# Kernel tuning notes

Measured on AMD Instinct MI355X. Metric: run time of the kernel, lower is better.

## Reference

```python
import jax, jax.numpy as jnp
import numpy as np


def setup_inputs() -> dict:
    key = jax.random.key(0)
    kK, kP, ki, ke = jax.random.split(key, 4)
    B, n = 512, 4096
    K_batch = jax.random.normal(kK, (B, n), dtype=jnp.float32)
    # Phi must be symmetric PSD (the module treats it as a kernel/metric matrix:
    # grad of sum(R@A*R) is written as 2*R@A, valid only for symmetric A).
    W = jax.random.normal(kP, (n, n), dtype=jnp.float32) / np.float32(np.sqrt(n))
    Phi = W @ W.T  # eigenvalues O(1)
    imp = jax.random.normal(ki, (1024,), dtype=jnp.float32)
    exc = jax.random.normal(ke, (1024,), dtype=jnp.float32)
    a = jnp.float32(1.0)
    gamma = jnp.float32(1.0)
    return {"K_batch": K_batch, "a": a, "exc": exc, "imp": imp,
            "Phi": Phi, "gamma": gamma}


def reference(K_batch, a, exc, imp, Phi, gamma):
    """OptNet-style layer: solve, per sample i,
         min_r  (gamma/B)*||r||^2 + ((||imp||^2+||exc||^2)/B) * r^T Phi r
         s.t.   a * <r, k_i> = 1
    Closed-form KKT solution (what the original SPG iteration converges to):
         r_i = M^{-1} k_i / (a * k_i^T M^{-1} k_i),
         M   = (gamma/B) I + ((||imp||^2+||exc||^2)/B) Phi.
    """
    B, n = K_batch.shape
    imp2 = jnp.sum(imp * imp)   # ||imp||^2
    exc2 = jnp.sum(exc * exc)   # ||exc||^2
    M = (imp2 + exc2) / B * Phi + (gamma / B) * jnp.eye(n, dtype=K_batch.dtype)
    # z_i = M^{-1} k_i for all samples at once: solve with B right-hand sides.
    Z = jnp.linalg.solve(M, K_batch.T).T            # [B, n]
    denom = a * jnp.sum(Z * K_batch, axis=1)        # [B], = a * k_i^T M^{-1} k_i
    opt_x = Z / denom[:, None]                      # [B, n]
    return opt_x
```

## Files before the change

### kernel.cpp

```cpp
#include <hip/hip_runtime.h>


#define N    4096
#define NRHS 512
#define NB   128
#define PSTR 68
#define DSTR 136
#define TSTR 136
#define BSTR 68

__device__ __forceinline__ int xcd_map(int bid, int nwg) {
  int x = bid & 7, i = bid >> 3;
  int q = nwg >> 3, r = nwg & 7;
  return (x < r ? x * (q + 1) : r * (q + 1) + (x - r) * q) + i;
}

template<int S>
__device__ __forceinline__ void asm_levelA(float* __restrict__ sh, int tid) {
  constexpr int TOT = (64 / S) * S * (S / 4);
  constexpr int F4 = S / 4;
  for (int id = tid; id < TOT; id += 512) {
    int pair = id / (S * F4);
    int rem = id - pair * (S * F4);
    int r = rem / F4, c4 = rem - r * F4;
    int o = 2 * S * pair;
    const float* arow = &sh[(o + S + r) * DSTR + o];
    float4 a4 = {0.f, 0.f, 0.f, 0.f};
    for (int t = 0; t < S; ++t) {
      float a = arow[t];
      const float4 b = *(const float4*)&sh[(o + t) * DSTR + o + 4 * c4];
      a4.x += a * b.x; a4.y += a * b.y; a4.z += a * b.z; a4.w += a * b.w;
    }
    *(float4*)&sh[(S * pair + r) * DSTR + 64 + 4 * c4] = a4;
  }
}
template<int S>
__device__ __forceinline__ void asm_levelB(float* __restrict__ sh, int tid) {
  constexpr int TOT = (64 / S) * S * (S / 4);
  constexpr int F4 = S / 4;
  for (int id = tid; id < TOT; id += 512) {
    int pair = id / (S * F4);
    int rem = id - pair * (S * F4);
    int r = rem / F4, c4 = rem - r * F4;
    int o = 2 * S * pair;
    const float* u2row = &sh[(o + S + r) * DSTR + o + S];
    float4 a4 = {0.f, 0.f, 0.f, 0.f};
    for (int t = 0; t < S; ++t) {
      float a = u2row[t];
      const float4 w = *(const float4*)&sh[(S * pair + t) * DSTR + 64 + 4 * c4];
      a4.x += a * w.x; a4.y += a * w.y; a4.z += a * w.z; a4.w += a * w.w;
    }
    float4 ov = {-a4.x, -a4.y, -a4.z, -a4.w};
    *(float4*)&sh[(o + S + r) * DSTR + o + 4 * c4] = ov;
  }
}

__global__ __launch_bounds__(256) void k_scalars(const float* __restrict__ imp,
                                                 const float* __restrict__ exc,
                                                 const float* __restrict__ gamma,
                                                 float* __restrict__ c) {
  __shared__ float red[256];
  int tid = threadIdx.x;
  float s = 0.0f;
  for (int i = tid; i < 1024; i += 256) { float x = imp[i], y = exc[i]; s += x * x + y * y; }
  red[tid] = s; __syncthreads();
  for (int w = 128; w > 0; w >>= 1) { if (tid < w) red[tid] += red[tid + w]; __syncthreads(); }
  if (tid == 0) { c[0] = red[0] / 512.0f; c[1] = gamma[0] / 512.0f; }
}

__global__ __launch_bounds__(256) void k_build_M(const float* __restrict__ Phi,
                                                 const float* __restrict__ c,
                                                 float* __restrict__ M) {
  int idx = blockIdx.x * 256 + threadIdx.x;
  int base = idx * 4;
  float4 p = *(const float4*)(Phi + base);
  float c1 = c[0], c2 = c[1];
  float4 m;
  m.x = c1 * p.x; m.y = c1 * p.y; m.z = c1 * p.z; m.w = c1 * p.w;
  int r = base >> 12, c0 = base & (N - 1);
  if (r == c0)     m.x += c2;
  if (r == c0 + 1) m.y += c2;
  if (r == c0 + 2) m.z += c2;
  if (r == c0 + 3) m.w += c2;
  *(float4*)(M + base) = m;
}

__global__ __launch_bounds__(256) void k_transpose(const float* __restrict__ K,
                                                   float* __restrict__ S) {
  __shared__ float t[32][33];
  int bi = blockIdx.x, bb = blockIdx.y;
  int tx = threadIdx.x & 31, ty = threadIdx.x >> 5;
  for (int r = 0; r < 4; ++r)
    t[ty + 8 * r][tx] = K[(size_t)(bb * 32 + ty + 8 * r) * N + bi * 32 + tx];
  __syncthreads();
  for (int r = 0; r < 4; ++r)
    S[(size_t)(bi * 32 + ty + 8 * r) * NRHS + bb * 32 + tx] = t[tx][ty + 8 * r];
}

__global__ __launch_bounds__(512, 2) void k_syrk_potrf(float* __restrict__ M,
                                                       float* __restrict__ U,
                                                       int kdiag, int k0) {
  __shared__ float sh[NB * DSTR];
  __shared__ float dinv[NB];
  float* Pa = sh;
  float* Pb = sh + NB * PSTR;
  int tid = threadIdx.x;
  int p = (gridDim.x > 1) ? xcd_map(blockIdx.x, gridDim.x) : 0;
  int g4 = tid >> 4;
  int cm = tid & 15;
  int rr4 = g4 * 4;

  if (p > 0) {
    int br = (int)((sqrtf(8.f * (float)p + 1.f) - 1.f) * 0.5f);
    while (((br + 1) * (br + 2)) / 2 <= p) ++br;
    while ((br * (br + 1)) / 2 > p) --br;
    int bc = p - (br * (br + 1)) / 2;
    int t0k = kdiag * NB;
    int r0 = t0k + br * NB, c0 = t0k + bc * NB;
    float acc[4][8] = {};
    for (int ch = 0; ch < 2; ++ch) {
      int kc = k0 + ch * 64;
      __syncthreads();
#pragma unroll
      for (int i = 0; i < 4; ++i) {
        int idx = tid + (i << 9);
        int r = idx >> 4, f4 = idx & 15;
        *(float4*)&Pa[r * PSTR + 4 * f4] = *(const float4*)(M + (size_t)(r0 + r) * N + kc + 4 * f4);
        *(float4*)&Pb[r * PSTR + 4 * f4] = *(const float4*)(M + (size_t)(c0 + r) * N + kc + 4 * f4);
      }
      __syncthreads();
#pragma unroll 2
      for (int tc = 0; tc < 64; tc += 4) {
        float4 a4[4], b4[8];
#pragma unroll
        for (int q = 0; q < 4; ++q) a4[q] = *(const float4*)&Pa[(rr4 + ((q + g4) & 3)) * PSTR + tc];
#pragma unroll
        for (int w = 0; w < 8; ++w) b4[w] = *(const float4*)&Pb[(cm + 16 * w) * PSTR + tc];
#pragma unroll
        for (int q = 0; q < 4; ++q)
#pragma unroll
          for (int w = 0; w < 8; ++w)
            acc[q][w] += a4[q].x * b4[w].x + a4[q].y * b4[w].y
                       + a4[q].z * b4[w].z + a4[q].w * b4[w].w;
      }
    }
    for (int q = 0; q < 4; ++q) {
      int row = r0 + rr4 + ((q + g4) & 3);
      float* mp = M + (size_t)row * N + c0 + cm;
#pragma unroll
      for (int w = 0; w < 8; ++w) mp[16 * w] -= acc[q][w];
    }
    return;
  }

  int kr = kdiag * NB;
  float acc[4][8] = {};
  if (k0 >= 0) {
    for (int ch = 0; ch < 2; ++ch) {
      int kc = k0 + ch * 64;
      __syncthreads();
#pragma unroll
      for (int i = 0; i < 4; ++i) {
        int idx = tid + (i << 9);
        int r = idx >> 4, f4 = idx & 15;
        *(float4*)&Pa[r * PSTR + 4 * f4] = *(const float4*)(M + (size_t)(kr + r) * N + kc + 4 * f4);
      }
      __syncthreads();
#pragma unroll 2
      for (int tc = 0; tc < 64; tc += 4) {
        float4 a4[4], b4[8];
#pragma unroll
        for (int q = 0; q < 4; ++q) a4[q] = *(const float4*)&Pa[(rr4 + ((q + g4) & 3)) * PSTR + tc];
#pragma unroll
        for (int w = 0; w < 8; ++w) b4[w] = *(const float4*)&Pa[(cm + 16 * w) * PSTR + tc];
#pragma unroll
        for (int q = 0; q < 4; ++q)
#pragma unroll
          for (int w = 0; w < 8; ++w)
            acc[q][w] += a4[q].x * b4[w].x + a4[q].y * b4[w].y
                       + a4[q].z * b4[w].z + a4[q].w * b4[w].w;
      }
    }
  }
  __syncthreads();
#pragma unroll
  for (int e = 0; e < 8; ++e) {
    int idx = tid + (e << 9);
    int r = idx >> 5, f4 = idx & 31;
    *(float4*)&sh[r * DSTR + 4 * f4] = *(const float4*)(M + (size_t)(kr + r) * N + kr + 4 * f4);
  }
  __syncthreads();
#pragma unroll
  for (int q = 0; q < 4; ++q) {
    int row = rr4 + ((q + g4) & 3);
#pragma unroll
    for (int w = 0; w < 8; ++w) {
      int col = cm + 16 * w;
      if ((row >> 4) < (col >> 4)) sh[row * DSTR + col] = 0.0f;
      else if (k0 >= 0) sh[row * DSTR + col] -= acc[q][w];
    }
  }
  __syncthreads();

#pragma unroll 1
  for (int pp = 0; pp < 8; ++pp) {
    const int b0 = 16 * pp;
    if (tid < 16) {
      int l = tid;
      float r[16];
#pragma unroll
      for (int t = 0; t < 16; ++t) r[t] = sh[(b0 + l) * DSTR + b0 + t];
#pragma unroll
      for (int j = 0; j < 16; ++j) {
        float d = __shfl(r[j], j);
        float inv = rsqrtf(d);
        if (l == j) r[j] = d * inv;
        else if (l > j) r[j] *= inv;
        if (l == 0) dinv[b0 + j] = inv;
#pragma unroll
        for (int t = j + 1; t < 16; ++t) {
          float Ltj = __shfl(r[j], t);
          if (l >= t) r[t] -= r[j] * Ltj;
        }
      }
#pragma unroll
      for (int t = 0; t < 16; ++t) if (t <= l) sh[(b0 + l) * DSTR + b0 + t] = r[t];
    }
    __syncthreads();
    const int base = b0 + 16, nbl = NB - base;
    if (nbl > 0) {
      if (tid < nbl) {
        const int rg = base + tid;
        float xr[16];
#pragma unroll
        for (int j = 0; j < 16; ++j) {
          float v = sh[rg * DSTR + b0 + j];
#pragma unroll
          for (int t = 0; t < 16; ++t)
            if (t < j) v -= xr[t] * sh[(b0 + j) * DSTR + b0 + t];
          xr[j] = v * dinv[b0 + j];
          sh[rg * DSTR + b0 + j] = xr[j];
        }
      }
      __syncthreads();
      for (int i = tid >> 3; i < nbl; i += 64) {
        const float* ai = &sh[(base + i) * DSTR + b0];
        float4 a0 = *(const float4*)ai,       a1 = *(const float4*)(ai + 4);
        float4 a2 = *(const float4*)(ai + 8), a3 = *(const float4*)(ai + 12);
        for (int j = tid & 7; j <= i; j += 8) {
          const float* bj = &sh[(base + j) * DSTR + b0];
          float4 c0 = *(const float4*)bj,       c1 = *(const float4*)(bj + 4);
          float4 c2 = *(const float4*)(bj + 8), c3 = *(const float4*)(bj + 12);
          float s = a0.x*c0.x + a0.y*c0.y + a0.z*c0.z + a0.w*c0.w
                  + a1.x*c1.x + a1.y*c1.y + a1.z*c1.z + a1.w*c1.w
                  + a2.x*c2.x + a2.y*c2.y + a2.z*c2.z + a2.w*c2.w
                  + a3.x*c3.x + a3.y*c3.y + a3.z*c3.z + a3.w*c3.w;
          sh[(base + i) * DSTR + base + j] -= s;
        }
      }
      __syncthreads();
    }
  }

  if (tid < 128) {
    const int g = tid >> 4, l = tid & 15, b0 = 16 * g;
    float x[16];
#pragma unroll
    for (int i = 0; i < 16; ++i) {
      float s = (l == i) ? 1.0f : 0.0f;
#pragma unroll
      for (int t = 0; t < 16; ++t)
        if (t < i) s -= sh[(b0 + i) * DSTR + b0 + t] * x[t];
      x[i] = s * dinv[b0 + i];
      sh[(b0 + i) * DSTR + b0 + l] = x[i];
    }
  }
  __syncthreads();

  asm_levelA<16>(sh, tid); __syncthreads();
  asm_levelB<16>(sh, tid); __syncthreads();
  asm_levelA<32>(sh, tid); __syncthreads();
  asm_levelB<32>(sh, tid); __syncthreads();
  asm_levelA<64>(sh, tid); __syncthreads();
  asm_levelB<64>(sh, tid); __syncthreads();

#pragma unroll
  for (int e = 0; e < 8; ++e) {
    int idx = tid + (e << 9);
    int i = idx >> 5, f4 = idx & 31;
    float4 v;
    if ((i >> 4) >= (f4 >> 2)) v = *(const float4*)&sh[i * DSTR + 4 * f4];
    else v = make_float4(0.f, 0.f, 0.f, 0.f);
    *(float4*)(U + (size_t)i * NB + 4 * f4) = v;
  }
}

__global__ __launch_bounds__(512, 2) void k_trsm(float* __restrict__ M,
                                                 const float* __restrict__ Ug, int k0) {
  __shared__ float Pa[NB * PSTR];
  __shared__ float Pb[NB * PSTR];
  int tid = threadIdx.x;
  int g4 = tid >> 4, rr4 = g4 * 4, cm = tid & 15;
  int r0 = k0 + NB + blockIdx.x * NB;
  float acc[4][8] = {};
  for (int ch = 0; ch < 2; ++ch) {
    int kc = k0 + ch * 64;
    __syncthreads();
#pragma unroll
    for (int i = 0; i < 4; ++i) {
      int idx = tid + (i << 9);
      int r = idx >> 4, f4 = idx & 15;
      *(float4*)&Pa[r * PSTR + 4 * f4] = *(const float4*)(M + (size_t)(r0 + r) * N + kc + 4 * f4);
      *(float4*)&Pb[r * PSTR + 4 * f4] = *(const float4*)(Ug + (size_t)r * NB + ch * 64 + 4 * f4);
    }
    __syncthreads();
#pragma unroll 2
    for (int tc = 0; tc < 64; tc += 4) {
      float4 a4[4], b4[8];
#pragma unroll
      for (int q = 0; q < 4; ++q) a4[q] = *(const float4*)&Pa[(rr4 + ((q + g4) & 3)) * PSTR + tc];
#pragma unroll
      for (int w = 0; w < 8; ++w) b4[w] = *(const float4*)&Pb[(cm + 16 * w) * PSTR + tc];
#pragma unroll
      for (int q = 0; q < 4; ++q)
#pragma unroll
        for (int w = 0; w < 8; ++w)
          acc[q][w] += a4[q].x * b4[w].x + a4[q].y * b4[w].y
                     + a4[q].z * b4[w].z + a4[q].w * b4[w].w;
    }
  }
  for (int q = 0; q < 4; ++q) {
    int row = r0 + rr4 + ((q + g4) & 3);
    float* mp = M + (size_t)row * N + k0 + cm;
#pragma unroll
    for (int w = 0; w < 8; ++w) mp[16 * w] = acc[q][w];
  }
}

__global__ __launch_bounds__(256) void k_fsolve(float* __restrict__ S,
                                                float* __restrict__ X,
                                                const float* __restrict__ M,
                                                const float* __restrict__ Uk,
                                                int k0) {
  __shared__ float Xl[NB][BSTR];
  __shared__ float Aa[16][TSTR];
  __shared__ float Bb[16][BSTR];
  int tid = threadIdx.x;
  int id = xcd_map(blockIdx.x, gridDim.x);
  int d = id >> 3;
  int b0 = (id & 7) * 64;
  int i0g = k0 + d * NB;
  int ii = (tid >> 3) * 4, bl = (tid & 7) * 8;
  float acc[4][8] = {};
  for (int tch = 0; tch < NB; tch += 16) {
#pragma unroll
    for (int it = 0; it < 2; ++it) {
      int idx = tid + it * 256;
      int j = idx >> 2, f4 = idx & 3;
      const float4 v = *(const float4*)(Uk + (size_t)j * NB + tch + 4 * f4);
      Aa[4 * f4 + 0][j] = v.x; Aa[4 * f4 + 1][j] = v.y;
      Aa[4 * f4 + 2][j] = v.z; Aa[4 * f4 + 3][j] = v.w;
    }
    {
      int t = tid >> 4, f = tid & 15;
      *(float4*)&Bb[t][4 * f] = *(const float4*)(S + (size_t)(k0 + tch + t) * NRHS + b0 + 4 * f);
    }
    __syncthreads();
#pragma unroll 4
    for (int t = 0; t < 16; ++t) {
      float4 a0 = *(const float4*)&Aa[t][ii];
      float4 b0v = *(const float4*)&Bb[t][bl];
      float4 b1v = *(const float4*)&Bb[t][bl + 4];
      float av[4] = {a0.x, a0.y, a0.z, a0.w};
      float bv[8] = {b0v.x, b0v.y, b0v.z, b0v.w, b1v.x, b1v.y, b1v.z, b1v.w};
#pragma unroll
      for (int q = 0; q < 4; ++q)
#pragma unroll
        for (int w = 0; w < 8; ++w) acc[q][w] += av[q] * bv[w];
    }
    __syncthreads();
  }
  if (d == 0) {
    for (int q = 0; q < 4; ++q) {
      float* xp = X + (size_t)(k0 + ii + q) * NRHS + b0 + bl;
      float4 x0 = {acc[q][0], acc[q][1], acc[q][2], acc[q][3]};
      float4 x1 = {acc[q][4], acc[q][5], acc[q][6], acc[q][7]};
      *(float4*)xp = x0; *((float4*)xp + 1) = x1;
    }
    return;
  }
  for (int q = 0; q < 4; ++q) {
    float4 x0 = {acc[q][0], acc[q][1], acc[q][2], acc[q][3]};
    float4 x1 = {acc[q][4], acc[q][5], acc[q][6], acc[q][7]};
    *(float4*)&Xl[ii + q][bl] = x0; *(float4*)&Xl[ii + q][bl + 4] = x1;
  }
  __syncthreads();
  float acc2[4][8] = {};
  for (int tch = 0; tch < NB; tch += 16) {
    for (int idx = tid; idx < 512; idx += 256) {
      int r = idx >> 2, q = idx & 3;
      const float4 v = *(const float4*)(M + (size_t)(i0g + r) * N + k0 + tch + 4 * q);
      Aa[4 * q + 0][r] = v.x; Aa[4 * q + 1][r] = v.y;
      Aa[4 * q + 2][r] = v.z; Aa[4 * q + 3][r] = v.w;
    }
    __syncthreads();
#pragma unroll 4
    for (int t = 0; t < 16; ++t) {
      float4 a0 = *(const float4*)&Aa[t][ii];
      float4 b0v = *(const float4*)&Xl[tch + t][bl];
      float4 b1v = *(const float4*)&Xl[tch + t][bl + 4];
      float av[4] = {a0.x, a0.y, a0.z, a0.w};
      float bv[8] = {b0v.x, b0v.y, b0v.z, b0v.w, b1v.x, b1v.y, b1v.z, b1v.w};
#pragma unroll
      for (int q = 0; q < 4; ++q)
#pragma unroll
        for (int w = 0; w < 8; ++w) acc2[q][w] += av[q] * bv[w];
    }
    __syncthreads();
  }
  for (int q = 0; q < 4; ++q) {
    float* sp = S + (size_t)(i0g + ii + q) * NRHS + b0 + bl;
    float4 x0 = *(float4*)sp, x1 = *((float4*)sp + 1);
    x0.x -= acc2[q][0]; x0.y -= acc2[q][1]; x0.z -= acc2[q][2]; x0.w -= acc2[q][3];
    x1.x -= acc2[q][4]; x1.y -= acc2[q][5]; x1.z -= acc2[q][6]; x1.w -= acc2[q][7];
    *(float4*)sp = x0; *((float4*)sp + 1) = x1;
  }
}

__global__ __launch_bounds__(256) void k_bsolve(float* __restrict__ X,
                                                float* __restrict__ S,
                                                const float* __restrict__ M,
                                                const float* __restrict__ Uk,
                                                int k0) {
  __shared__ float Xl[NB][BSTR];
  __shared__ float Aa[16][TSTR];
  __shared__ float Bb[16][BSTR];
  int tid = threadIdx.x;
  int id = xcd_map(blockIdx.x, gridDim.x);
  int d = id >> 3;
  int b0 = (id & 7) * 64;
  int i0g = k0 - d * NB;
  int ii = (tid >> 3) * 4, bl = (tid & 7) * 8;
  float acc[4][8] = {};
  for (int tch = 0; tch < NB; tch += 16) {
    for (int idx = tid; idx < 512; idx += 256) {
      int t = idx >> 5, f = idx & 31;
      *(float4*)&Aa[t][4 * f] = *(const float4*)(Uk + (size_t)(tch + t) * NB + 4 * f);
    }
    {
      int t = tid >> 4, f = tid & 15;
      *(float4*)&Bb[t][4 * f] = *(const float4*)(X + (size_t)(k0 + tch + t) * NRHS + b0 + 4 * f);
    }
    __syncthreads();
#pragma unroll 4
    for (int t = 0; t < 16; ++t) {
      float4 a0 = *(const float4*)&Aa[t][ii];
      float4 b0v = *(const float4*)&Bb[t][bl];
      float4 b1v = *(const float4*)&Bb[t][bl + 4];
      float av[4] = {a0.x, a0.y, a0.z, a0.w};
      float bv[8] = {b0v.x, b0v.y, b0v.z, b0v.w, b1v.x, b1v.y, b1v.z, b1v.w};
#pragma unroll
      for (int q = 0; q < 4; ++q)
#pragma unroll
        for (int w = 0; w < 8; ++w) acc[q][w] += av[q] * bv[w];
    }
    __syncthreads();
  }
  if (d == 0) {
    for (int q = 0; q < 4; ++q) {
      float* sp = S + (size_t)(k0 + ii + q) * NRHS + b0 + bl;
      float4 x0 = {acc[q][0], acc[q][1], acc[q][2], acc[q][3]};
      float4 x1 = {acc[q][4], acc[q][5], acc[q][6], acc[q][7]};
      *(float4*)sp = x0; *((float4*)sp + 1) = x1;
    }
    return;
  }
  for (int q = 0; q < 4; ++q) {
    float4 x0 = {acc[q][0], acc[q][1], acc[q][2], acc[q][3]};
    float4 x1 = {acc[q][4], acc[q][5], acc[q][6], acc[q][7]};
    *(float4*)&Xl[ii + q][bl] = x0; *(float4*)&Xl[ii + q][bl + 4] = x1;
  }
  __syncthreads();
  float acc2[4][8] = {};
  for (int tch = 0; tch < NB; tch += 16) {
    for (int idx = tid; idx < 512; idx += 256) {
      int t = idx >> 5, f = idx & 31;
      *(float4*)&Aa[t][4 * f] = *(const float4*)(M + (size_t)(k0 + tch + t) * N + i0g + 4 * f);
    }
    __syncthreads();
#pragma unroll 4
    for (int t = 0; t < 16; ++t) {
      float4 a0 = *(const float4*)&Aa[t][ii];
      float4 b0v = *(const float4*)&Xl[tch + t][bl];
      float4 b1v = *(const float4*)&Xl[tch + t][bl + 4];
      float av[4] = {a0.x, a0.y, a0.z, a0.w};
      float bv[8] = {b0v.x, b0v.y, b0v.z, b0v.w, b1v.x, b1v.y, b1v.z, b1v.w};
#pragma unroll
      for (int q = 0; q < 4; ++q)
#pragma unroll
        for (int w = 0; w < 8; ++w) acc2[q][w] += av[q] * bv[w];
    }
    __syncthreads();
  }
  for (int q = 0; q < 4; ++q) {
    float* xp = X + (size_t)(i0g + ii + q) * NRHS + b0 + bl;
    float4 x0 = *(float4*)xp, x1 = *((float4*)xp + 1);
    x0.x -= acc2[q][0]; x0.y -= acc2[q][1]; x0.z -= acc2[q][2]; x0.w -= acc2[q][3];
    x1.x -= acc2[q][4]; x1.y -= acc2[q][5]; x1.z -= acc2[q][6]; x1.w -= acc2[q][7];
    *(float4*)xp = x0; *((float4*)xp + 1) = x1;
  }
}

__global__ __launch_bounds__(256) void k_final(const float* __restrict__ S,
                                               const float* __restrict__ K,
                                               const float* __restrict__ a_ptr,
                                               float* __restrict__ out) {
  __shared__ float red[256];
  int b = blockIdx.x, tid = threadIdx.x;
  float s = 0.0f;
  for (int i = tid; i < N; i += 256) s += S[(size_t)i * NRHS + b] * K[(size_t)b * N + i];
  red[tid] = s; __syncthreads();
  for (int w = 128; w > 0; w >>= 1) { if (tid < w) red[tid] += red[tid + w]; __syncthreads(); }
  float inv = 1.0f / (a_ptr[0] * red[0]);
  for (int i = tid; i < N; i += 256) out[(size_t)b * N + i] = S[(size_t)i * NRHS + b] * inv;
}

extern "C" void kernel_launch(void* const* d_in, const int* in_sizes, int n_in,
                              void* d_out, int out_size, void* d_ws, size_t ws_size,
                              hipStream_t stream) {
  const float* Kb    = (const float*)d_in[0];
  const float* a     = (const float*)d_in[1];
  const float* exc   = (const float*)d_in[2];
  const float* imp   = (const float*)d_in[3];
  const float* Phi   = (const float*)d_in[4];
  const float* gamma = (const float*)d_in[5];
  float* out = (float*)d_out;

  float* M  = (float*)d_ws;
  float* S  = M + (size_t)N * N;
  float* X  = S + (size_t)N * NRHS;
  float* U  = X + (size_t)N * NRHS;
  float* c  = U + (size_t)32 * NB * NB;

  k_scalars<<<1, 256, 0, stream>>>(imp, exc, gamma, c);
  k_build_M<<<N * N / 1024, 256, 0, stream>>>(Phi, c, M);
  k_transpose<<<dim3(N / 32, NRHS / 32), 256, 0, stream>>>(Kb, S);

  k_syrk_potrf<<<1, 512, 0, stream>>>(M, U, 0, -1);
  for (int k = 0; k <= 30; ++k) {
    int k0 = k * NB;
    k_trsm<<<31 - k, 512, 0, stream>>>(M, U + (size_t)k * NB * NB, k0);
    int T = 31 - k;
    int pairs = (T * (T + 1)) / 2;
    k_syrk_potrf<<<pairs, 512, 0, stream>>>(M, U + (size_t)(k + 1) * NB * NB, k + 1, k0);
  }
  for (int k = 0; k < 32; ++k)
    k_fsolve<<<8 * (32 - k), 256, 0, stream>>>(S, X, M, U + (size_t)k * NB * NB, k * NB);
  for (int k = 31; k >= 0; --k)
    k_bsolve<<<8 * (k + 1), 256, 0, stream>>>(X, S, M, U + (size_t)k * NB * NB, k * NB);
  k_final<<<NRHS, 256, 0, stream>>>(S, Kb, a, out);
}
```

Baseline: 4.976 ms.

## Use 32-wide panels in diagonal-block Cholesky and overlap next corner factor with trailing update

The in-LDS factorization of each 128x128 diagonal block now works on 32-column panels instead of 16. Each step runs the next panel's corner factorization on one wavefront while the other threads apply the remaining trailing update in parallel. The diagonal-block inverse starts from 32x32 blocks, which removes the 16-level assembly passes. The goal is fewer barriers and less serial work on the critical path per block. The cost is larger per-thread register arrays (32 floats) and longer serial triangular solves per thread.

New measurement: 5.319 ms. 6.9% more time.

```diff
diff --git a/kernel.cpp b/kernel.cpp
--- a/kernel.cpp
+++ b/kernel.cpp
@@ -55,6 +55,42 @@
   }
 }
 
+__device__ __forceinline__ void corner_factor32(float* __restrict__ sh,
+                                                float* __restrict__ dinv,
+                                                int c0, int l) {
+  float r[32];
+#pragma unroll
+  for (int t = 0; t < 32; ++t) r[t] = sh[(c0 + l) * DSTR + c0 + t];
+#pragma unroll
+  for (int j = 0; j < 32; ++j) {
+    float d = __shfl(r[j], j);
+    float inv = rsqrtf(d);
+    if (l == j) r[j] = d * inv;
+    else if (l > j) r[j] *= inv;
+    if (l == 0) dinv[c0 + j] = inv;
+#pragma unroll
+    for (int t = j + 1; t < 32; ++t) {
+      float Ltj = __shfl(r[j], t);
+      if (l >= t) r[t] -= r[j] * Ltj;
+    }
+  }
+#pragma unroll
+  for (int t = 0; t < 32; ++t) if (t <= l) sh[(c0 + l) * DSTR + c0 + t] = r[t];
+}
+
+__device__ __forceinline__ float dot32(const float* __restrict__ sh, int i, int j, int b0) {
+  const float* ai = &sh[i * DSTR + b0];
+  const float* bj = &sh[j * DSTR + b0];
+  float s = 0.0f;
+#pragma unroll
+  for (int q = 0; q < 8; ++q) {
+    float4 a = *(const float4*)(ai + 4 * q);
+    float4 b = *(const float4*)(bj + 4 * q);
+    s += a.x * b.x + a.y * b.y + a.z * b.z + a.w * b.w;
+  }
+  return s;
+}
+
 __global__ __launch_bounds__(256) void k_scalars(const float* __restrict__ imp,
                                                  const float* __restrict__ exc,
                                                  const float* __restrict__ gamma,
@@ -202,83 +238,65 @@
   }
   __syncthreads();
 
+  if (tid < 32) corner_factor32(sh, dinv, 0, tid);
+  __syncthreads();
 #pragma unroll 1
-  for (int pp = 0; pp < 8; ++pp) {
-    const int b0 = 16 * pp;
-    if (tid < 16) {
-      int l = tid;
-      float r[16];
-#pragma unroll
-      for (int t = 0; t < 16; ++t) r[t] = sh[(b0 + l) * DSTR + b0 + t];
-#pragma unroll
-      for (int j = 0; j < 16; ++j) {
-        float d = __shfl(r[j], j);
-        float inv = rsqrtf(d);
-        if (l == j) r[j] = d * inv;
-        else if (l > j) r[j] *= inv;
-        if (l == 0) dinv[b0 + j] = inv;
-#pragma unroll
-        for (int t = j + 1; t < 16; ++t) {
-          float Ltj = __shfl(r[j], t);
-          if (l >= t) r[t] -= r[j] * Ltj;
+  for (int pp = 0; pp < 3; ++pp) {
+    const int b0 = 32 * pp;
+    const int base = b0 + 32;
+    const int nbl = NB - base;
+    if (tid < nbl) {
+      const int rg = base + tid;
+      float xr[32];
+#pragma unroll
+      for (int j = 0; j < 32; ++j) {
+        float v = sh[rg * DSTR + b0 + j];
+#pragma unroll
+        for (int t = 0; t < 32; ++t)
+          if (t < j) v -= xr[t] * sh[(b0 + j) * DSTR + b0 + t];
+        xr[j] = v * dinv[b0 + j];
+        sh[rg * DSTR + b0 + j] = xr[j];
+      }
+    }
+    __syncthreads();
+    for (int e = tid; e < 1024; e += 512) {
+      int i = base + (e >> 5), j = base + (e & 31);
+      if (j <= i) sh[i * DSTR + j] -= dot32(sh, i, j, b0);
+    }
+    __syncthreads();
+    if (tid < 32) {
+      corner_factor32(sh, dinv, base, tid);
+    } else if (tid >= 64) {
+      const int base2 = base + 32;
+      const int nb2 = NB - base2;
+      if (nb2 > 0) {
+        const int ncol = NB - base;
+        const int tot = nb2 * ncol;
+        for (int e = tid - 64; e < tot; e += 448) {
+          int i = base2 + e / ncol;
+          int j = base + (e - (e / ncol) * ncol);
+          if (j <= i) sh[i * DSTR + j] -= dot32(sh, i, j, b0);
         }
       }
-#pragma unroll
-      for (int t = 0; t < 16; ++t) if (t <= l) sh[(b0 + l) * DSTR + b0 + t] = r[t];
-    }
-    __syncthreads();
-    const int base = b0 + 16, nbl = NB - base;
-    if (nbl > 0) {
-      if (tid < nbl) {
-        const int rg = base + tid;
-        float xr[16];
-#pragma unroll
-        for (int j = 0; j < 16; ++j) {
-          float v = sh[rg * DSTR + b0 + j];
-#pragma unroll
-          for (int t = 0; t < 16; ++t)
-            if (t < j) v -= xr[t] * sh[(b0 + j) * DSTR + b0 + t];
-          xr[j] = v * dinv[b0 + j];
-          sh[rg * DSTR + b0 + j] = xr[j];
-        }
-      }
-      __syncthreads();
-      for (int i = tid >> 3; i < nbl; i += 64) {
-        const float* ai = &sh[(base + i) * DSTR + b0];
-        float4 a0 = *(const float4*)ai,       a1 = *(const float4*)(ai + 4);
-        float4 a2 = *(const float4*)(ai + 8), a3 = *(const float4*)(ai + 12);
-        for (int j = tid & 7; j <= i; j += 8) {
-          const float* bj = &sh[(base + j) * DSTR + b0];
-          float4 c0 = *(const float4*)bj,       c1 = *(const float4*)(bj + 4);
-          float4 c2 = *(const float4*)(bj + 8), c3 = *(const float4*)(bj + 12);
-          float s = a0.x*c0.x + a0.y*c0.y + a0.z*c0.z + a0.w*c0.w
-                  + a1.x*c1.x + a1.y*c1.y + a1.z*c1.z + a1.w*c1.w
-                  + a2.x*c2.x + a2.y*c2.y + a2.z*c2.z + a2.w*c2.w
-                  + a3.x*c3.x + a3.y*c3.y + a3.z*c3.z + a3.w*c3.w;
-          sh[(base + i) * DSTR + base + j] -= s;
-        }
-      }
-      __syncthreads();
-    }
+    }
+    __syncthreads();
   }
 
   if (tid < 128) {
-    const int g = tid >> 4, l = tid & 15, b0 = 16 * g;
-    float x[16];
-#pragma unroll
-    for (int i = 0; i < 16; ++i) {
+    const int g = tid >> 5, l = tid & 31, c0 = 32 * g;
+    float x[32];
+#pragma unroll
+    for (int i = 0; i < 32; ++i) {
       float s = (l == i) ? 1.0f : 0.0f;
 #pragma unroll
-      for (int t = 0; t < 16; ++t)
-        if (t < i) s -= sh[(b0 + i) * DSTR + b0 + t] * x[t];
-      x[i] = s * dinv[b0 + i];
-      sh[(b0 + i) * DSTR + b0 + l] = x[i];
-    }
-  }
-  __syncthreads();
-
-  asm_levelA<16>(sh, tid); __syncthreads();
-  asm_levelB<16>(sh, tid); __syncthreads();
+      for (int t = 0; t < 32; ++t)
+        if (t < i) s -= sh[(c0 + i) * DSTR + c0 + t] * x[t];
+      x[i] = s * dinv[c0 + i];
+      sh[(c0 + i) * DSTR + c0 + l] = x[i];
+    }
+  }
+  __syncthreads();
+
   asm_levelA<32>(sh, tid); __syncthreads();
   asm_levelB<32>(sh, tid); __syncthreads();
   asm_levelA<64>(sh, tid); __syncthreads();
```

## Fuse triangular solve sweeps into persistent cooperative kernels with grid sync

Applied to the files above, without the earlier changes.

Replaces the 32 forward and 32 backward solve launches with one cooperative kernel each, which loops over block steps and uses grid.sync between them. Blocks that have no work at a given step stay idle until the next barrier. This removes per-launch overhead and launch gaps across 64 small kernels, at the cost of grid-wide barriers, a fixed 256-block grid that leaves more blocks idle in late steps, and dropping the XCD-aware block remapping.

Measured after the change: 6.724 ms. 1.35x slower.

```diff
diff --git a/kernel.cpp b/kernel.cpp
--- a/kernel.cpp
+++ b/kernel.cpp
@@ -1,4 +1,6 @@
 #include <hip/hip_runtime.h>
+#include <hip/hip_cooperative_groups.h>
+namespace cg = cooperative_groups;
 
 
 #define N    4096
@@ -337,177 +339,191 @@
   }
 }
 
-__global__ __launch_bounds__(256) void k_fsolve(float* __restrict__ S,
-                                                float* __restrict__ X,
-                                                const float* __restrict__ M,
-                                                const float* __restrict__ Uk,
-                                                int k0) {
+__global__ __launch_bounds__(256) void k_fsolve_coop(float* __restrict__ S,
+                                                     float* __restrict__ X,
+                                                     const float* __restrict__ M,
+                                                     const float* __restrict__ Uall) {
+  cg::grid_group grid = cg::this_grid();
   __shared__ float Xl[NB][BSTR];
   __shared__ float Aa[16][TSTR];
   __shared__ float Bb[16][BSTR];
   int tid = threadIdx.x;
-  int id = xcd_map(blockIdx.x, gridDim.x);
-  int d = id >> 3;
-  int b0 = (id & 7) * 64;
-  int i0g = k0 + d * NB;
+  int d = blockIdx.x >> 3;
+  int b0 = (blockIdx.x & 7) * 64;
   int ii = (tid >> 3) * 4, bl = (tid & 7) * 8;
-  float acc[4][8] = {};
-  for (int tch = 0; tch < NB; tch += 16) {
-#pragma unroll
-    for (int it = 0; it < 2; ++it) {
-      int idx = tid + it * 256;
-      int j = idx >> 2, f4 = idx & 3;
-      const float4 v = *(const float4*)(Uk + (size_t)j * NB + tch + 4 * f4);
-      Aa[4 * f4 + 0][j] = v.x; Aa[4 * f4 + 1][j] = v.y;
-      Aa[4 * f4 + 2][j] = v.z; Aa[4 * f4 + 3][j] = v.w;
-    }
-    {
-      int t = tid >> 4, f = tid & 15;
-      *(float4*)&Bb[t][4 * f] = *(const float4*)(S + (size_t)(k0 + tch + t) * NRHS + b0 + 4 * f);
-    }
-    __syncthreads();
+#pragma unroll 1
+  for (int k = 0; k < 32; ++k) {
+    if (d <= 31 - k) {
+      const float* Uk = Uall + (size_t)k * NB * NB;
+      const int k0 = k * NB;
+      const int i0g = k0 + d * NB;
+      float acc[4][8] = {};
+      for (int tch = 0; tch < NB; tch += 16) {
+#pragma unroll
+        for (int it = 0; it < 2; ++it) {
+          int idx = tid + it * 256;
+          int j = idx >> 2, f4 = idx & 3;
+          const float4 v = *(const float4*)(Uk + (size_t)j * NB + tch + 4 * f4);
+          Aa[4 * f4 + 0][j] = v.x; Aa[4 * f4 + 1][j] = v.y;
+          Aa[4 * f4 + 2][j] = v.z; Aa[4 * f4 + 3][j] = v.w;
+        }
+        {
+          int t = tid >> 4, f = tid & 15;
+          *(float4*)&Bb[t][4 * f] = *(const float4*)(S + (size_t)(k0 + tch + t) * NRHS + b0 + 4 * f);
+        }
+        __syncthreads();
 #pragma unroll 4
-    for (int t = 0; t < 16; ++t) {
-      float4 a0 = *(const float4*)&Aa[t][ii];
-      float4 b0v = *(const float4*)&Bb[t][bl];
-      float4 b1v = *(const float4*)&Bb[t][bl + 4];
-      float av[4] = {a0.x, a0.y, a0.z, a0.w};
-      float bv[8] = {b0v.x, b0v.y, b0v.z, b0v.w, b1v.x, b1v.y, b1v.z, b1v.w};
-#pragma unroll
-      for (int q = 0; q < 4; ++q)
-#pragma unroll
-        for (int w = 0; w < 8; ++w) acc[q][w] += av[q] * bv[w];
-    }
-    __syncthreads();
-  }
-  if (d == 0) {
-    for (int q = 0; q < 4; ++q) {
-      float* xp = X + (size_t)(k0 + ii + q) * NRHS + b0 + bl;
-      float4 x0 = {acc[q][0], acc[q][1], acc[q][2], acc[q][3]};
-      float4 x1 = {acc[q][4], acc[q][5], acc[q][6], acc[q][7]};
-      *(float4*)xp = x0; *((float4*)xp + 1) = x1;
-    }
-    return;
-  }
-  for (int q = 0; q < 4; ++q) {
-    float4 x0 = {acc[q][0], acc[q][1], acc[q][2], acc[q][3]};
-    float4 x1 = {acc[q][4], acc[q][5], acc[q][6], acc[q][7]};
-    *(float4*)&Xl[ii + q][bl] = x0; *(float4*)&Xl[ii + q][bl + 4] = x1;
-  }
-  __syncthreads();
-  float acc2[4][8] = {};
-  for (int tch = 0; tch < NB; tch += 16) {
-    for (int idx = tid; idx < 512; idx += 256) {
-      int r = idx >> 2, q = idx & 3;
-      const float4 v = *(const float4*)(M + (size_t)(i0g + r) * N + k0 + tch + 4 * q);
-      Aa[4 * q + 0][r] = v.x; Aa[4 * q + 1][r] = v.y;
-      Aa[4 * q + 2][r] = v.z; Aa[4 * q + 3][r] = v.w;
-    }
-    __syncthreads();
+        for (int t = 0; t < 16; ++t) {
+          float4 a0 = *(const float4*)&Aa[t][ii];
+          float4 b0v = *(const float4*)&Bb[t][bl];
+          float4 b1v = *(const float4*)&Bb[t][bl + 4];
+          float av[4] = {a0.x, a0.y, a0.z, a0.w};
+          float bv[8] = {b0v.x, b0v.y, b0v.z, b0v.w, b1v.x, b1v.y, b1v.z, b1v.w};
+#pragma unroll
+          for (int q = 0; q < 4; ++q)
+#pragma unroll
+            for (int w = 0; w < 8; ++w) acc[q][w] += av[q] * bv[w];
+        }
+        __syncthreads();
+      }
+      if (d == 0) {
+        for (int q = 0; q < 4; ++q) {
+          float* xp = X + (size_t)(k0 + ii + q) * NRHS + b0 + bl;
+          float4 x0 = {acc[q][0], acc[q][1], acc[q][2], acc[q][3]};
+          float4 x1 = {acc[q][4], acc[q][5], acc[q][6], acc[q][7]};
+          *(float4*)xp = x0; *((float4*)xp + 1) = x1;
+        }
+      } else {
+        for (int q = 0; q < 4; ++q) {
+          float4 x0 = {acc[q][0], acc[q][1], acc[q][2], acc[q][3]};
+          float4 x1 = {acc[q][4], acc[q][5], acc[q][6], acc[q][7]};
+          *(float4*)&Xl[ii + q][bl] = x0; *(float4*)&Xl[ii + q][bl + 4] = x1;
+        }
+        __syncthreads();
+        float acc2[4][8] = {};
+        for (int tch = 0; tch < NB; tch += 16) {
+          for (int idx = tid; idx < 512; idx += 256) {
+            int r = idx >> 2, q = idx & 3;
+            const float4 v = *(const float4*)(M + (size_t)(i0g + r) * N + k0 + tch + 4 * q);
+            Aa[4 * q + 0][r] = v.x; Aa[4 * q + 1][r] = v.y;
+            Aa[4 * q + 2][r] = v.z; Aa[4 * q + 3][r] = v.w;
+          }
+          __syncthreads();
 #pragma unroll 4
-    for (int t = 0; t < 16; ++t) {
-      float4 a0 = *(const float4*)&Aa[t][ii];
-      float4 b0v = *(const float4*)&Xl[tch + t][bl];
-      float4 b1v = *(const float4*)&Xl[tch + t][bl + 4];
-      float av[4] = {a0.x, a0.y, a0.z, a0.w};
-      float bv[8] = {b0v.x, b0v.y, b0v.z, b0v.w, b1v.x, b1v.y, b1v.z, b1v.w};
-#pragma unroll
-      for (int q = 0; q < 4; ++q)
-#pragma unroll
-        for (int w = 0; w < 8; ++w) acc2[q][w] += av[q] * bv[w];
-    }
-    __syncthreads();
-  }
-  for (int q = 0; q < 4; ++q) {
-    float* sp = S + (size_t)(i0g + ii + q) * NRHS + b0 + bl;
-    float4 x0 = *(float4*)sp, x1 = *((float4*)sp + 1);
-    x0.x -= acc2[q][0]; x0.y -= acc2[q][1]; x0.z -= acc2[q][2]; x0.w -= acc2[q][3];
-    x1.x -= acc2[q][4]; x1.y -= acc2[q][5]; x1.z -= acc2[q][6]; x1.w -= acc2[q][7];
-    *(float4*)sp = x0; *((float4*)sp + 1) = x1;
-  }
-}
-
-__global__ __launch_bounds__(256) void k_bsolve(float* __restrict__ X,
-                                                float* __restrict__ S,
-                                                const float* __restrict__ M,
-                                                const float* __restrict__ Uk,
-                                                int k0) {
+          for (int t = 0; t < 16; ++t) {
+            float4 a0 = *(const float4*)&Aa[t][ii];
+            float4 b0v = *(const float4*)&Xl[tch + t][bl];
+            float4 b1v = *(const float4*)&Xl[tch + t][bl + 4];
+            float av[4] = {a0.x, a0.y, a0.z, a0.w};
+            float bv[8] = {b0v.x, b0v.y, b0v.z, b0v.w, b1v.x, b1v.y, b1v.z, b1v.w};
+#pragma unroll
+            for (int q = 0; q < 4; ++q)
+#pragma unroll
+              for (int w = 0; w < 8; ++w) acc2[q][w] += av[q] * bv[w];
+          }
+          __syncthreads();
+        }
+        for (int q = 0; q < 4; ++q) {
+          float* sp = S + (size_t)(i0g + ii + q) * NRHS + b0 + bl;
+          float4 x0 = *(float4*)sp, x1 = *((float4*)sp + 1);
+          x0.x -= acc2[q][0]; x0.y -= acc2[q][1]; x0.z -= acc2[q][2]; x0.w -= acc2[q][3];
+          x1.x -= acc2[q][4]; x1.y -= acc2[q][5]; x1.z -= acc2[q][6]; x1.w -= acc2[q][7];
+          *(float4*)sp = x0; *((float4*)sp + 1) = x1;
+        }
+      }
+    }
+    grid.sync();
+  }
+}
+
+__global__ __launch_bounds__(256) void k_bsolve_coop(float* __restrict__ X,
+                                                     float* __restrict__ S,
+                                                     const float* __restrict__ M,
+                                                     const float* __restrict__ Uall) {
+  cg::grid_group grid = cg::this_grid();
   __shared__ float Xl[NB][BSTR];
   __shared__ float Aa[16][TSTR];
   __shared__ float Bb[16][BSTR];
   int tid = threadIdx.x;
-  int id = xcd_map(blockIdx.x, gridDim.x);
-  int d = id >> 3;
-  int b0 = (id & 7) * 64;
-  int i0g = k0 - d * NB;
+  int d = blockIdx.x >> 3;
+  int b0 = (blockIdx.x & 7) * 64;
   int ii = (tid >> 3) * 4, bl = (tid & 7) * 8;
-  float acc[4][8] = {};
-  for (int tch = 0; tch < NB; tch += 16) {
-    for (int idx = tid; idx < 512; idx += 256) {
-      int t = idx >> 5, f = idx & 31;
-      *(float4*)&Aa[t][4 * f] = *(const float4*)(Uk + (size_t)(tch + t) * NB + 4 * f);
-    }
-    {
-      int t = tid >> 4, f = tid & 15;
-      *(float4*)&Bb[t][4 * f] = *(const float4*)(X + (size_t)(k0 + tch + t) * NRHS + b0 + 4 * f);
-    }
-    __syncthreads();
+#pragma unroll 1
+  for (int k = 31; k >= 0; --k) {
+    if (d <= k) {
+      const float* Uk = Uall + (size_t)k * NB * NB;
+      const int k0 = k * NB;
+      const int i0g = k0 - d * NB;
+      float acc[4][8] = {};
+      for (int tch = 0; tch < NB; tch += 16) {
+        for (int idx = tid; idx < 512; idx += 256) {
+          int t = idx >> 5, f = idx & 31;
+          *(float4*)&Aa[t][4 * f] = *(const float4*)(Uk + (size_t)(tch + t) * NB + 4 * f);
+        }
+        {
+          int t = tid >> 4, f = tid & 15;
+          *(float4*)&Bb[t][4 * f] = *(const float4*)(X + (size_t)(k0 + tch + t) * NRHS + b0 + 4 * f);
+        }
+        __syncthreads();
 #pragma unroll 4
-    for (int t = 0; t < 16; ++t) {
-      float4 a0 = *(const float4*)&Aa[t][ii];
-      float4 b0v = *(const float4*)&Bb[t][bl];
-      float4 b1v = *(const float4*)&Bb[t][bl + 4];
-      float av[4] = {a0.x, a0.y, a0.z, a0.w};
-      float bv[8] = {b0v.x, b0v.y, b0v.z, b0v.w, b1v.x, b1v.y, b1v.z, b1v.w};
-#pragma unroll
-      for (int q = 0; q < 4; ++q)
-#pragma unroll
-        for (int w = 0; w < 8; ++w) acc[q][w] += av[q] * bv[w];
-    }
-    __syncthreads();
-  }
-  if (d == 0) {
-    for (int q = 0; q < 4; ++q) {
-      float* sp = S + (size_t)(k0 + ii + q) * NRHS + b0 + bl;
-      float4 x0 = {acc[q][0], acc[q][1], acc[q][2], acc[q][3]};
-      float4 x1 = {acc[q][4], acc[q][5], acc[q][6], acc[q][7]};
-      *(float4*)sp = x0; *((float4*)sp + 1) = x1;
-    }
-    return;
-  }
-  for (int q = 0; q < 4; ++q) {
-    float4 x0 = {acc[q][0], acc[q][1], acc[q][2], acc[q][3]};
-    float4 x1 = {acc[q][4], acc[q][5], acc[q][6], acc[q][7]};
-    *(float4*)&Xl[ii + q][bl] = x0; *(float4*)&Xl[ii + q][bl + 4] = x1;
-  }
-  __syncthreads();
-  float acc2[4][8] = {};
-  for (int tch = 0; tch < NB; tch += 16) {
-    for (int idx = tid; idx < 512; idx += 256) {
-      int t = idx >> 5, f = idx & 31;
-      *(float4*)&Aa[t][4 * f] = *(const float4*)(M + (size_t)(k0 + tch + t) * N + i0g + 4 * f);
-    }
-    __syncthreads();
+        for (int t = 0; t < 16; ++t) {
+          float4 a0 = *(const float4*)&Aa[t][ii];
+          float4 b0v = *(const float4*)&Bb[t][bl];
+          float4 b1v = *(const float4*)&Bb[t][bl + 4];
+          float av[4] = {a0.x, a0.y, a0.z, a0.w};
+          float bv[8] = {b0v.x, b0v.y, b0v.z, b0v.w, b1v.x, b1v.y, b1v.z, b1v.w};
+#pragma unroll
+          for (int q = 0; q < 4; ++q)
+#pragma unroll
+            for (int w = 0; w < 8; ++w) acc[q][w] += av[q] * bv[w];
+        }
+        __syncthreads();
+      }
+      if (d == 0) {
+        for (int q = 0; q < 4; ++q) {
+          float* sp = S + (size_t)(k0 + ii + q) * NRHS + b0 + bl;
+          float4 x0 = {acc[q][0], acc[q][1], acc[q][2], acc[q][3]};
+          float4 x1 = {acc[q][4], acc[q][5], acc[q][6], acc[q][7]};
+          *(float4*)sp = x0; *((float4*)sp + 1) = x1;
+        }
+      } else {
+        for (int q = 0; q < 4; ++q) {
+          float4 x0 = {acc[q][0], acc[q][1], acc[q][2], acc[q][3]};
+          float4 x1 = {acc[q][4], acc[q][5], acc[q][6], acc[q][7]};
+          *(float4*)&Xl[ii + q][bl] = x0; *(float4*)&Xl[ii + q][bl + 4] = x1;
+        }
+        __syncthreads();
+        float acc2[4][8] = {};
+        for (int tch = 0; tch < NB; tch += 16) {
+          for (int idx = tid; idx < 512; idx += 256) {
+            int t = idx >> 5, f = idx & 31;
+            *(float4*)&Aa[t][4 * f] = *(const float4*)(M + (size_t)(k0 + tch + t) * N + i0g + 4 * f);
+          }
+          __syncthreads();
 #pragma unroll 4
-    for (int t = 0; t < 16; ++t) {
-      float4 a0 = *(const float4*)&Aa[t][ii];
-      float4 b0v = *(const float4*)&Xl[tch + t][bl];
-      float4 b1v = *(const float4*)&Xl[tch + t][bl + 4];
-      float av[4] = {a0.x, a0.y, a0.z, a0.w};
-      float bv[8] = {b0v.x, b0v.y, b0v.z, b0v.w, b1v.x, b1v.y, b1v.z, b1v.w};
-#pragma unroll
-      for (int q = 0; q < 4; ++q)
-#pragma unroll
-        for (int w = 0; w < 8; ++w) acc2[q][w] += av[q] * bv[w];
-    }
-    __syncthreads();
-  }
-  for (int q = 0; q < 4; ++q) {
-    float* xp = X + (size_t)(i0g + ii + q) * NRHS + b0 + bl;
-    float4 x0 = *(float4*)xp, x1 = *((float4*)xp + 1);
-    x0.x -= acc2[q][0]; x0.y -= acc2[q][1]; x0.z -= acc2[q][2]; x0.w -= acc2[q][3];
-    x1.x -= acc2[q][4]; x1.y -= acc2[q][5]; x1.z -= acc2[q][6]; x1.w -= acc2[q][7];
-    *(float4*)xp = x0; *((float4*)xp + 1) = x1;
+          for (int t = 0; t < 16; ++t) {
+            float4 a0 = *(const float4*)&Aa[t][ii];
+            float4 b0v = *(const float4*)&Xl[tch + t][bl];
+            float4 b1v = *(const float4*)&Xl[tch + t][bl + 4];
+            float av[4] = {a0.x, a0.y, a0.z, a0.w};
+            float bv[8] = {b0v.x, b0v.y, b0v.z, b0v.w, b1v.x, b1v.y, b1v.z, b1v.w};
+#pragma unroll
+            for (int q = 0; q < 4; ++q)
+#pragma unroll
+              for (int w = 0; w < 8; ++w) acc2[q][w] += av[q] * bv[w];
+          }
+          __syncthreads();
+        }
+        for (int q = 0; q < 4; ++q) {
+          float* xp = X + (size_t)(i0g + ii + q) * NRHS + b0 + bl;
+          float4 x0 = *(float4*)xp, x1 = *((float4*)xp + 1);
+          x0.x -= acc2[q][0]; x0.y -= acc2[q][1]; x0.z -= acc2[q][2]; x0.w -= acc2[q][3];
+          x1.x -= acc2[q][4]; x1.y -= acc2[q][5]; x1.z -= acc2[q][6]; x1.w -= acc2[q][7];
+          *(float4*)xp = x0; *((float4*)xp + 1) = x1;
+        }
+      }
+    }
+    grid.sync();
   }
 }
 
@@ -554,9 +570,14 @@
     int pairs = (T * (T + 1)) / 2;
     k_syrk_potrf<<<pairs, 512, 0, stream>>>(M, U + (size_t)(k + 1) * NB * NB, k + 1, k0);
   }
-  for (int k = 0; k < 32; ++k)
-    k_fsolve<<<8 * (32 - k), 256, 0, stream>>>(S, X, M, U + (size_t)k * NB * NB, k * NB);
-  for (int k = 31; k >= 0; --k)
-    k_bsolve<<<8 * (k + 1), 256, 0, stream>>>(X, S, M, U + (size_t)k * NB * NB, k * NB);
+
+  {
+    float* Sp = S; float* Xp = X;
+    const float* Mp = M; const float* Up = U;
+    void* fa[4] = { (void*)&Sp, (void*)&Xp, (void*)&Mp, (void*)&Up };
+    hipLaunchCooperativeKernel((const void*)k_fsolve_coop, dim3(256), dim3(256), fa, 0, stream);
+    void* ba[4] = { (void*)&Xp, (void*)&Sp, (void*)&Mp, (void*)&Up };
+    hipLaunchCooperativeKernel((const void*)k_bsolve_coop, dim3(256), dim3(256), ba, 0, stream);
+  }
   k_final<<<NRHS, 256, 0, stream>>>(S, Kb, a, out);
 }
```
